# Kernel optimization log

Hardware: AMD Instinct MI355X
Metric: run time of the kernel (lower is better)

## Reference

```python
import jax, jax.numpy as jnp
import numpy as np

B, T, C = 4, 2048, 1024
H, HS = 16, 64


def setup_inputs() -> dict:
    key = jax.random.key(0)
    ks = jax.random.split(key, 5)
    scale = (H * C) ** (-0.5)
    x = jax.random.normal(ks[0], (B, T, C), dtype=jnp.float32)
    Wk = jax.random.normal(ks[1], (H, C, HS), dtype=jnp.float32) * scale
    Wq = jax.random.normal(ks[2], (H, C, HS), dtype=jnp.float32) * scale
    Wv = jax.random.normal(ks[3], (H, C, HS), dtype=jnp.float32) * scale
    proj_w = jax.random.normal(ks[4], (C, C), dtype=jnp.float32) / C ** 0.5
    proj_b = jnp.zeros((C,), dtype=jnp.float32)
    return {"x": x, "Wk": Wk, "Wq": Wq, "Wv": Wv, "proj_w": proj_w, "proj_b": proj_b}


def reference(x, Wk, Wq, Wv, proj_w, proj_b):
    b, t, c = x.shape
    # per-head projections: (B,T,C) x (H,C,D) -> (B,H,T,D)
    q = jnp.einsum('btc,hcd->bhtd', x, Wq)
    k = jnp.einsum('btc,hcd->bhtd', x, Wk)
    v = jnp.einsum('btc,hcd->bhtd', x, Wv)
    # NOTE: original module does not scale by 1/sqrt(head_size)
    wei = jnp.einsum('bhtd,bhsd->bhts', q, k)  # (B,H,T,T)
    causal = jnp.tril(jnp.ones((t, t), dtype=bool))
    wei = jnp.where(causal, wei, -jnp.inf)
    wei = jax.nn.softmax(wei, axis=-1)
    out = jnp.einsum('bhts,bhsd->bhtd', wei, v)
    out = out.transpose(0, 2, 1, 3).reshape(b, t, c)  # concat heads
    return out @ proj_w + proj_b
```

## Files before the change

### kernel.cpp

```cpp
#include <hip/hip_runtime.h>

typedef unsigned short u16;
typedef u16 u16x4 __attribute__((ext_vector_type(4)));
typedef u16 u16x8 __attribute__((ext_vector_type(8)));
typedef unsigned u32x2 __attribute__((ext_vector_type(2)));
typedef __bf16 bf16x8 __attribute__((ext_vector_type(8)));
typedef float f32x4 __attribute__((ext_vector_type(4)));

#define DEV static __device__ __forceinline__

DEV u16 f2bf(float f) {
  union { float f; unsigned u; } v; v.f = f;
  return (u16)((v.u + 0x7FFFu + ((v.u >> 16) & 1u)) >> 16);
}

DEV unsigned pack2(float a, float b) {
  unsigned ua = __builtin_bit_cast(unsigned, a) + 0x8000u;
  unsigned ub = __builtin_bit_cast(unsigned, b) + 0x8000u;
  return (ua >> 16) | (ub & 0xFFFF0000u);
}

DEV void async16(const void* g, void* l) {
  __builtin_amdgcn_global_load_lds((const __attribute__((address_space(1))) void*)g,
                                   (__attribute__((address_space(3))) void*)l, 16, 0, 0);
}

DEV f32x4 mfma16(bf16x8 a, bf16x8 b, f32x4 c) {
  return __builtin_amdgcn_mfma_f32_16x16x32_bf16(a, b, c, 0, 0, 0);
}

DEV float exp2fast(float x) { return __builtin_amdgcn_exp2f(x); }

__global__ __launch_bounds__(256) void k_prep(const float* __restrict__ x,
                                              const float* __restrict__ Wk,
                                              const float* __restrict__ Wq,
                                              const float* __restrict__ Wv,
                                              const float* __restrict__ pw,
                                              u16* __restrict__ xb,
                                              u16* __restrict__ wT,
                                              u16* __restrict__ pwT) {
  __shared__ float t[64 * 72];
  const int bid = blockIdx.x, tid = threadIdx.x;
  if (bid < 8192) {
    int i = bid * 1024 + tid * 4;
    float4 v = *(const float4*)(x + i);
    u16x4 o = { f2bf(v.x), f2bf(v.y), f2bf(v.z), f2bf(v.w) };
    *(u16x4*)(xb + i) = o;
    return;
  }
  const int role = bid - 8192;
  const float* src;
  u16* dst;
  int rows, cols, bx, by, bz;
  float scale;
  if (role < 768) {
    const int w = role >> 8, rem = role & 255;
    src = (w == 0) ? Wq : ((w == 1) ? Wk : Wv);
    dst = wT + (size_t)w * 1024 * 1024;
    scale = (w == 0) ? 1.44269504088896340736f : 1.0f;
    rows = 1024; cols = 64; bx = 0; by = rem >> 4; bz = rem & 15;
  } else {
    const int p = role - 768;
    src = pw; dst = pwT; scale = 1.0f;
    rows = 1024; cols = 1024; bx = p & 15; by = p >> 4; bz = 0;
  }
  src += (size_t)bz * rows * cols;
  dst += (size_t)bz * rows * cols;
  const int c0 = bx * 64, r0 = by * 64;
  const int rr = tid >> 2, cb = (tid & 3) * 16;
  const float* s = src + (size_t)(r0 + rr) * cols + c0 + cb;
  float4 v0 = *(const float4*)(s + 0);
  float4 v1 = *(const float4*)(s + 4);
  float4 v2 = *(const float4*)(s + 8);
  float4 v3 = *(const float4*)(s + 12);
  *(float4*)(t + rr * 72 + cb + 0)  = v0;
  *(float4*)(t + rr * 72 + cb + 4)  = v1;
  *(float4*)(t + rr * 72 + cb + 8)  = v2;
  *(float4*)(t + rr * 72 + cb + 12) = v3;
  __syncthreads();
  const int dd = tid >> 2, eb = (tid & 3) * 16;
  u16x8 o0, o1;
#pragma unroll
  for (int e = 0; e < 8; ++e) o0[e] = f2bf(t[(eb + e) * 72 + dd] * scale);
#pragma unroll
  for (int e = 0; e < 8; ++e) o1[e] = f2bf(t[(eb + 8 + e) * 72 + dd] * scale);
  u16* dp = dst + (size_t)(c0 + dd) * rows + r0 + eb;
  *(u16x8*)dp = o0;
  *(u16x8*)(dp + 8) = o1;
}

template <int MODE>
__global__ __launch_bounds__(256) void k_gemm(const u16* __restrict__ A,
                                              const u16* __restrict__ Bt,
                                              u16* __restrict__ qd,
                                              u16* __restrict__ kd,
                                              u16* __restrict__ vd,
                                              float* __restrict__ out,
                                              const float* __restrict__ bias) {
  __shared__ u16 As[128 * 64];
  __shared__ u16 Bs[128 * 64];
  const int tid = threadIdx.x;
  const int wave = tid >> 6, lane = tid & 63;
  const int quad = lane >> 4, l15 = lane & 15;
  const int wm = wave & 1, wn = wave >> 1;
  const size_t mb = blockIdx.y, nb = blockIdx.x;

  const int lrow = lane >> 3;
  const int lchunk = ((lane & 7) ^ lrow) << 3;
  const u16* ga = A + (mb * 128 + wave * 32 + lrow) * 1024 + lchunk;
  const u16* gb = Bt + (nb * 128 + wave * 32 + lrow) * 1024 + lchunk;
  u16* adst = As + wave * 2048;
  u16* bdst = Bs + wave * 2048;

  const int sa0 = ((0 + quad) ^ (l15 & 7)) << 3;
  const int sa1 = ((4 + quad) ^ (l15 & 7)) << 3;

  f32x4 acc[4][4] = {};
  for (int k0 = 0; k0 < 1024; k0 += 64) {
#pragma unroll
    for (int m = 0; m < 4; ++m) {
      async16(ga + m * 8 * 1024, adst + m * 512);
      async16(gb + m * 8 * 1024, bdst + m * 512);
    }
    ga += 64; gb += 64;
    __syncthreads();
#pragma unroll
    for (int c = 0; c < 2; ++c) {
      const int swz = c ? sa1 : sa0;
      bf16x8 af[4], bf[4];
#pragma unroll
      for (int i = 0; i < 4; ++i)
        af[i] = *(const bf16x8*)(As + (wm * 64 + i * 16 + l15) * 64 + swz);
#pragma unroll
      for (int j = 0; j < 4; ++j)
        bf[j] = *(const bf16x8*)(Bs + (wn * 64 + j * 16 + l15) * 64 + swz);
#pragma unroll
      for (int i = 0; i < 4; ++i)
#pragma unroll
        for (int j = 0; j < 4; ++j)
          acc[i][j] = mfma16(af[i], bf[j], acc[i][j]);
    }
    __syncthreads();
  }

  const size_t m0 = mb * 128 + wm * 64;
  const int n0 = (int)nb * 128 + wn * 64;
  if (MODE == 0) {
#pragma unroll
    for (int j = 0; j < 4; ++j) {
      const int n = n0 + j * 16 + l15;
      const int p = n >> 10, hh = (n >> 6) & 15, d = n & 63;
      if (p == 2) {
#pragma unroll
        for (int i = 0; i < 4; ++i) {
          const size_t m = m0 + i * 16 + quad * 4;
          const size_t bb = m >> 11, tt = m & 2047;
          u16x4 pk = { f2bf(acc[i][j][0]), f2bf(acc[i][j][1]),
                       f2bf(acc[i][j][2]), f2bf(acc[i][j][3]) };
          *(u16x4*)(vd + ((bb * 16 + hh) * 64 + d) * 2048 + tt) = pk;
        }
      } else {
        u16* dst = (p == 0) ? qd : kd;
#pragma unroll
        for (int i = 0; i < 4; ++i)
#pragma unroll
          for (int r = 0; r < 4; ++r) {
            const size_t m = m0 + i * 16 + quad * 4 + r;
            const size_t bb = m >> 11, tt = m & 2047;
            dst[((bb * 16 + hh) * 2048 + tt) * 64 + d] = f2bf(acc[i][j][r]);
          }
      }
    }
  } else {
#pragma unroll
    for (int j = 0; j < 4; ++j) {
      const int n = n0 + j * 16 + l15;
      const float bv = bias[n];
#pragma unroll
      for (int i = 0; i < 4; ++i)
#pragma unroll
        for (int r = 0; r < 4; ++r) {
          const size_t m = m0 + i * 16 + quad * 4 + r;
          out[m * 1024 + n] = acc[i][j][r] + bv;
        }
    }
  }
}

__global__ __launch_bounds__(256) void k_attn(const u16* __restrict__ Qg,
                                              const u16* __restrict__ Kg,
                                              const u16* __restrict__ Vtg,
                                              u16* __restrict__ Og) {
  __shared__ u16 Kbuf[2 * 4096];
  __shared__ u16 Vbuf[2 * 4096];
  __shared__ u16 Pbuf[4 * 32 * 72];
  const int tid = threadIdx.x;
  const int wave = tid >> 6, lane = tid & 63;
  const int quad = lane >> 4, l15 = lane & 15;
  const int quad4 = quad * 4, quad8 = quad * 8;
  const int bh = blockIdx.x;
  const int qb = 15 - (int)blockIdx.y;
  const u16* kg = Kg + (size_t)bh * 2048 * 64;
  const u16* vg = Vtg + (size_t)bh * 64 * 2048;
  u16* Pw = Pbuf + wave * (32 * 72);
  const int b = bh >> 4, h = bh & 15;

  const int lrow = lane >> 3;
  const int lchunk = ((lane & 7) ^ lrow) << 3;
  const u16* kst = kg + (size_t)(wave * 16 + lrow) * 64 + lchunk;
  const u16* vst = vg + (size_t)(wave * 16 + lrow) * 2048 + lchunk;
  u16* kdst0 = Kbuf + wave * 1024;
  u16* vdst0 = Vbuf + wave * 1024;

  const int rowoff = l15 * 64;
  const int swz0 = ((0 + quad) ^ (l15 & 7)) << 3;
  const int swz1 = ((4 + quad) ^ (l15 & 7)) << 3;

  const int qlo = qb * 128 + wave * 32;
  const int ntw = 2 * qb + 1 + (wave >> 1);
  const int ntb = 2 * qb + 2;
  const u16* qg = Qg + ((size_t)bh * 2048 + (size_t)qb * 128) * 64;

  bf16x8 qf[2][2];
#pragma unroll
  for (int i = 0; i < 2; ++i)
#pragma unroll
    for (int c = 0; c < 2; ++c)
      qf[i][c] = *(const bf16x8*)(qg + (size_t)(wave * 32 + i * 16 + l15) * 64 +
                                  c * 32 + quad8);

  f32x4 oacc[2][4] = {};
  float lsum[2] = {0.f, 0.f};
  const f32x4 fzero = {};

  async16(kst, kdst0);
  async16(kst + 512, kdst0 + 512);
  async16(vst, vdst0);
  async16(vst + 16384, vdst0 + 512);

  for (int it = 0; it < ntb; ++it) {
    __syncthreads();

    if (it + 1 < ntb) {
      const int buf = (it + 1) & 1;
      const size_t s0n = (size_t)(it + 1) * 64;
      async16(kst + s0n * 64,       kdst0 + buf * 4096);
      async16(kst + s0n * 64 + 512, kdst0 + buf * 4096 + 512);
      async16(vst + s0n,            vdst0 + buf * 4096);
      async16(vst + s0n + 16384,    vdst0 + buf * 4096 + 512);
    }

    if (it < ntw) {
      const int s0 = it * 64;
      const u16* Kb = Kbuf + (it & 1) * 4096;
      const u16* Vb = Vbuf + (it & 1) * 4096;

      f32x4 sacc[4][2];
#pragma unroll
      for (int j = 0; j < 4; ++j) {
        bf16x8 kf0 = *(const bf16x8*)(Kb + j * 1024 + rowoff + swz0);
        bf16x8 kf1 = *(const bf16x8*)(Kb + j * 1024 + rowoff + swz1);
        sacc[j][0] = mfma16(kf0, qf[0][0], fzero);
        sacc[j][0] = mfma16(kf1, qf[0][1], sacc[j][0]);
        sacc[j][1] = mfma16(kf0, qf[1][0], fzero);
        sacc[j][1] = mfma16(kf1, qf[1][1], sacc[j][1]);
      }

#pragma unroll
      for (int j = 0; j < 4; ++j)
#pragma unroll
        for (int i = 0; i < 2; ++i)
#pragma unroll
          for (int r = 0; r < 4; ++r)
            sacc[j][i][r] = exp2fast(sacc[j][i][r]);

      if (it == ntw - 1) {
#pragma unroll
        for (int j = 0; j < 4; ++j)
#pragma unroll
          for (int i = 0; i < 2; ++i)
#pragma unroll
            for (int r = 0; r < 4; ++r)
              if (s0 + j * 16 + quad4 + r > qlo + i * 16 + l15) sacc[j][i][r] = 0.f;
      }

#pragma unroll
      for (int j = 0; j < 4; ++j)
#pragma unroll
        for (int i = 0; i < 2; ++i) {
          lsum[i] += (sacc[j][i][0] + sacc[j][i][1]) +
                     (sacc[j][i][2] + sacc[j][i][3]);
          u32x2 pk = { pack2(sacc[j][i][0], sacc[j][i][1]),
                       pack2(sacc[j][i][2], sacc[j][i][3]) };
          *(u32x2*)(Pw + (i * 16 + l15) * 72 + j * 16 + quad4) = pk;
        }

      bf16x8 pa[2][2];
#pragma unroll
      for (int i = 0; i < 2; ++i)
#pragma unroll
        for (int c = 0; c < 2; ++c)
          pa[i][c] = *(const bf16x8*)(Pw + (i * 16 + l15) * 72 + c * 32 + quad8);

#pragma unroll
      for (int n = 0; n < 4; ++n) {
        bf16x8 vf0 = *(const bf16x8*)(Vb + n * 1024 + rowoff + swz0);
        bf16x8 vf1 = *(const bf16x8*)(Vb + n * 1024 + rowoff + swz1);
        oacc[0][n] = mfma16(pa[0][0], vf0, oacc[0][n]);
        oacc[0][n] = mfma16(pa[0][1], vf1, oacc[0][n]);
        oacc[1][n] = mfma16(pa[1][0], vf0, oacc[1][n]);
        oacc[1][n] = mfma16(pa[1][1], vf1, oacc[1][n]);
      }
    }
  }

#pragma unroll
  for (int i = 0; i < 2; ++i) {
    lsum[i] += __shfl_xor(lsum[i], 16, 64);
    lsum[i] += __shfl_xor(lsum[i], 32, 64);
  }
#pragma unroll
  for (int i = 0; i < 2; ++i)
#pragma unroll
    for (int r = 0; r < 4; ++r) {
      const float inv = 1.0f / __shfl(lsum[i], quad4 + r, 16);
      const size_t t = (size_t)qb * 128 + wave * 32 + i * 16 + quad4 + r;
#pragma unroll
      for (int n = 0; n < 4; ++n)
        Og[((size_t)b * 2048 + t) * 1024 + h * 64 + n * 16 + l15] =
            f2bf(oacc[i][n][r] * inv);
    }
}

extern "C" void kernel_launch(void* const* d_in, const int* in_sizes, int n_in,
                              void* d_out, int out_size, void* d_ws, size_t ws_size,
                              hipStream_t stream) {
  const float* x  = (const float*)d_in[0];
  const float* Wk = (const float*)d_in[1];
  const float* Wq = (const float*)d_in[2];
  const float* Wv = (const float*)d_in[3];
  const float* pw = (const float*)d_in[4];
  const float* pb = (const float*)d_in[5];
  float* out = (float*)d_out;
  char* ws = (char*)d_ws;

  u16* xb  = (u16*)(ws + 0);
  u16* wT  = (u16*)(ws + 16777216);
  u16* pwT = (u16*)(ws + 23068672);
  u16* q   = (u16*)(ws + 25165824);
  u16* kb  = (u16*)(ws + 41943040);
  u16* vt  = (u16*)(ws + 58720256);
  u16* att = (u16*)(ws + 0);

  k_prep<<<9216, 256, 0, stream>>>(x, Wk, Wq, Wv, pw, xb, wT, pwT);
  k_gemm<0><<<dim3(24, 64), 256, 0, stream>>>(xb, wT, q, kb, vt, nullptr, nullptr);
  k_attn<<<dim3(64, 16), 256, 0, stream>>>(q, kb, vt, att);
  k_gemm<1><<<dim3(8, 64), 256, 0, stream>>>(att, pwT, nullptr, nullptr, nullptr, out, pb);
}
```

Before: 244.9 us.

## Restructure GEMM into 256x128 tiles with triple-buffered async LDS pipeline

Rewrites the bf16 GEMM kernel used for the QKV and output projections. Each block is now 512 threads computing a 256x128 tile, and K-tiles are loaded into a triple-buffered LDS ring two steps ahead, using explicit vmcnt waits, raw s_barrier and sched_barrier fences, and setprio around MFMA bursts. It also remaps block IDs to group workgroups, intended to improve L2 reuse. This aims to hide global load latency behind MFMA work and to halve redundant B-tile loads, at the cost of 144KB of LDS per block, which limits occupancy, and of fragile hand-placed synchronization.

After: 241.7 us. About the same (-1.3%).

```diff
diff --git a/kernel.cpp b/kernel.cpp
--- a/kernel.cpp
+++ b/kernel.cpp
@@ -30,6 +30,9 @@
 }
 
 DEV float exp2fast(float x) { return __builtin_amdgcn_exp2f(x); }
+
+#define BARRIER() asm volatile("s_barrier" ::: "memory")
+#define SB0() __builtin_amdgcn_sched_barrier(0)
 
 __global__ __launch_bounds__(256) void k_prep(const float* __restrict__ x,
                                               const float* __restrict__ Wk,
@@ -90,61 +93,102 @@
 }
 
 template <int MODE>
-__global__ __launch_bounds__(256) void k_gemm(const u16* __restrict__ A,
-                                              const u16* __restrict__ Bt,
-                                              u16* __restrict__ qd,
-                                              u16* __restrict__ kd,
-                                              u16* __restrict__ vd,
-                                              float* __restrict__ out,
-                                              const float* __restrict__ bias) {
-  __shared__ u16 As[128 * 64];
-  __shared__ u16 Bs[128 * 64];
+__global__ __launch_bounds__(512, 2) void k_gemm(const u16* __restrict__ A,
+                                                 const u16* __restrict__ Bt,
+                                                 u16* __restrict__ qd,
+                                                 u16* __restrict__ kd,
+                                                 u16* __restrict__ vd,
+                                                 float* __restrict__ out,
+                                                 const float* __restrict__ bias) {
+  __shared__ u16 lds[3 * 24576];
   const int tid = threadIdx.x;
-  const int wave = tid >> 6, lane = tid & 63;
+  const int w = tid >> 6, lane = tid & 63;
   const int quad = lane >> 4, l15 = lane & 15;
-  const int wm = wave & 1, wn = wave >> 1;
-  const size_t mb = blockIdx.y, nb = blockIdx.x;
-
-  const int lrow = lane >> 3;
-  const int lchunk = ((lane & 7) ^ lrow) << 3;
-  const u16* ga = A + (mb * 128 + wave * 32 + lrow) * 1024 + lchunk;
-  const u16* gb = Bt + (nb * 128 + wave * 32 + lrow) * 1024 + lchunk;
-  u16* adst = As + wave * 2048;
-  u16* bdst = Bs + wave * 2048;
-
-  const int sa0 = ((0 + quad) ^ (l15 & 7)) << 3;
-  const int sa1 = ((4 + quad) ^ (l15 & 7)) << 3;
+  const int wm = w >> 1, wn = w & 1;
+
+  const int gx = (int)gridDim.x;
+  int lin = (int)blockIdx.y * gx + (int)blockIdx.x;
+  const int nwg = gx * (int)gridDim.y;
+  lin = (lin & 7) * (nwg >> 3) + (lin >> 3);
+  const size_t mb = (size_t)(lin / gx);
+  const int nb = lin % gx;
+
+  const int lr = lane >> 3;
+  const int lc = ((lane & 7) ^ lr) << 3;
+  const u16* ga0 = A  + (mb * 256 + (size_t)(w * 8 + lr)) * 1024 + lc;
+  const u16* gb0 = Bt + ((size_t)nb * 128 + (size_t)(w * 8 + lr)) * 1024 + lc;
+
+  const int swz0 = ((0 + quad) ^ (l15 & 7)) << 3;
+  const int swz1 = ((4 + quad) ^ (l15 & 7)) << 3;
 
   f32x4 acc[4][4] = {};
-  for (int k0 = 0; k0 < 1024; k0 += 64) {
-#pragma unroll
-    for (int m = 0; m < 4; ++m) {
-      async16(ga + m * 8 * 1024, adst + m * 512);
-      async16(gb + m * 8 * 1024, bdst + m * 512);
-    }
-    ga += 64; gb += 64;
-    __syncthreads();
-#pragma unroll
-    for (int c = 0; c < 2; ++c) {
-      const int swz = c ? sa1 : sa0;
-      bf16x8 af[4], bf[4];
-#pragma unroll
-      for (int i = 0; i < 4; ++i)
-        af[i] = *(const bf16x8*)(As + (wm * 64 + i * 16 + l15) * 64 + swz);
-#pragma unroll
-      for (int j = 0; j < 4; ++j)
-        bf[j] = *(const bf16x8*)(Bs + (wn * 64 + j * 16 + l15) * 64 + swz);
-#pragma unroll
-      for (int i = 0; i < 4; ++i)
-#pragma unroll
-        for (int j = 0; j < 4; ++j)
-          acc[i][j] = mfma16(af[i], bf[j], acc[i][j]);
-    }
-    __syncthreads();
-  }
-
-  const size_t m0 = mb * 128 + wm * 64;
-  const int n0 = (int)nb * 128 + wn * 64;
+
+#pragma unroll
+  for (int s2 = 0; s2 < 2; ++s2) {
+    u16* d = lds + s2 * 24576 + w * 512;
+#pragma unroll
+    for (int g = 0; g < 4; ++g) async16(ga0 + (size_t)g * 65536 + s2 * 64, d + g * 4096);
+#pragma unroll
+    for (int g = 0; g < 2; ++g) async16(gb0 + (size_t)g * 65536 + s2 * 64, d + 16384 + g * 4096);
+  }
+  asm volatile("s_waitcnt vmcnt(6)" ::: "memory");
+  BARRIER(); SB0();
+
+#pragma unroll
+  for (int s = 0; s < 16; ++s) {
+    const u16* Ab = lds + (s % 3) * 24576;
+    const u16* Bb = Ab + 16384;
+
+    bf16x8 a0[4], b0[4];
+#pragma unroll
+    for (int i = 0; i < 4; ++i)
+      a0[i] = *(const bf16x8*)(Ab + (wm * 64 + i * 16 + l15) * 64 + swz0);
+#pragma unroll
+    for (int j = 0; j < 4; ++j)
+      b0[j] = *(const bf16x8*)(Bb + (wn * 64 + j * 16 + l15) * 64 + swz0);
+    if (s < 14) {
+      u16* d = lds + ((s + 2) % 3) * 24576 + w * 512;
+      async16(ga0 + 0 * 65536 + (s + 2) * 64, d + 0 * 4096);
+      async16(ga0 + 1 * 65536 + (s + 2) * 64, d + 1 * 4096);
+      async16(ga0 + 2 * 65536 + (s + 2) * 64, d + 2 * 4096);
+    }
+    SB0(); BARRIER(); SB0();
+    __builtin_amdgcn_s_setprio(1);
+#pragma unroll
+    for (int i = 0; i < 4; ++i)
+#pragma unroll
+      for (int j = 0; j < 4; ++j) acc[i][j] = mfma16(a0[i], b0[j], acc[i][j]);
+    __builtin_amdgcn_s_setprio(0);
+    SB0(); BARRIER(); SB0();
+
+    bf16x8 a1[4], b1[4];
+#pragma unroll
+    for (int i = 0; i < 4; ++i)
+      a1[i] = *(const bf16x8*)(Ab + (wm * 64 + i * 16 + l15) * 64 + swz1);
+#pragma unroll
+    for (int j = 0; j < 4; ++j)
+      b1[j] = *(const bf16x8*)(Bb + (wn * 64 + j * 16 + l15) * 64 + swz1);
+    if (s < 14) {
+      u16* d = lds + ((s + 2) % 3) * 24576 + w * 512;
+      async16(ga0 + 3 * 65536 + (s + 2) * 64, d + 3 * 4096);
+      async16(gb0 + 0 * 65536 + (s + 2) * 64, d + 16384 + 0 * 4096);
+      async16(gb0 + 1 * 65536 + (s + 2) * 64, d + 16384 + 4096);
+    }
+    SB0(); BARRIER(); SB0();
+    __builtin_amdgcn_s_setprio(1);
+#pragma unroll
+    for (int i = 0; i < 4; ++i)
+#pragma unroll
+      for (int j = 0; j < 4; ++j) acc[i][j] = mfma16(a1[i], b1[j], acc[i][j]);
+    __builtin_amdgcn_s_setprio(0);
+    SB0();
+    if (s < 14)       { asm volatile("s_waitcnt vmcnt(6)" ::: "memory"); }
+    else if (s == 14) { asm volatile("s_waitcnt vmcnt(0)" ::: "memory"); }
+    if (s < 15) { BARRIER(); SB0(); }
+  }
+
+  const size_t m0 = mb * 256 + wm * 64;
+  const int n0 = nb * 128 + wn * 64;
   if (MODE == 0) {
 #pragma unroll
     for (int j = 0; j < 4; ++j) {
@@ -353,7 +397,7 @@
   u16* att = (u16*)(ws + 0);
 
   k_prep<<<9216, 256, 0, stream>>>(x, Wk, Wq, Wv, pw, xb, wT, pwT);
-  k_gemm<0><<<dim3(24, 64), 256, 0, stream>>>(xb, wT, q, kb, vt, nullptr, nullptr);
+  k_gemm<0><<<dim3(24, 32), 512, 0, stream>>>(xb, wT, q, kb, vt, nullptr, nullptr);
   k_attn<<<dim3(64, 16), 256, 0, stream>>>(q, kb, vt, att);
-  k_gemm<1><<<dim3(8, 64), 256, 0, stream>>>(att, pwT, nullptr, nullptr, nullptr, out, pb);
-}
+  k_gemm<1><<<dim3(8, 32), 512, 0, stream>>>(att, pwT, nullptr, nullptr, nullptr, out, pb);
+}
```
